# Kernel optimization log

Measured on AMD Instinct MI355X. Metric: run time of the kernel, lower is better.

## Reference

```python
import jax, jax.numpy as jnp
import numpy as np

E = 8            # moe_num_experts
FFN = 8192       # ffn_hidden_size
D = 2048         # d_model
B, T = 1, 4096


def setup_inputs() -> dict:
    key = jax.random.key(0)
    k1, k2, k3, k4 = jax.random.split(key, 4)
    x = jax.random.normal(k1, (B, T, D), dtype=jnp.float32)
    # params stored flat as (E*FFN, D), as in the flax module
    w1 = jax.random.normal(k2, (E * FFN, D), dtype=jnp.float32) * 0.02
    v1 = jax.random.normal(k3, (E * FFN, D), dtype=jnp.float32) * 0.02
    w2 = jax.random.normal(k4, (E * FFN, D), dtype=jnp.float32) * 0.02
    return {"x": x, "w1": w1, "v1": v1, "w2": w2, "expert_idx": 3}


def reference(x, w1, v1, w2, expert_idx):
    # select this expert's weight slabs: (FFN, D) each
    expert_shape = (E, FFN, D)
    ew1 = w1.reshape(expert_shape)[expert_idx]
    ev1 = v1.reshape(expert_shape)[expert_idx]
    ew2 = w2.reshape(expert_shape)[expert_idx]
    # gate and up projections: [B,T,D] x [D,FFN] -> [B,T,FFN]
    x1 = jnp.einsum('btd,fd->btf', x, ew1)
    x2 = jnp.einsum('btd,fd->btf', x, ev1)
    h = jax.nn.silu(x1) * x2
    # down projection (note: matmul with ew2, i.e. contraction over FFN)
    out = jnp.einsum('btf,fd->btd', h, ew2)
    return out
```

## Files before the change

kernel.cpp:

```cpp
#include <hip/hip_runtime.h>

#define E_NUM 8
#define FFN_DIM 8192
#define D_DIM 2048
#define T_DIM 4096

using bf16x8 = __attribute__((ext_vector_type(8))) short;
using f32x4  = __attribute__((ext_vector_type(4))) float;
using u16x8  = __attribute__((ext_vector_type(8))) unsigned short;

__device__ __forceinline__ unsigned short f2bf(float f) {
  union { float f; unsigned int u; } v; v.f = f;
  unsigned int u = v.u;
  unsigned int r = (u + 0x7FFFu + ((u >> 16) & 1u)) >> 16;
  return (unsigned short)r;
}

__device__ __forceinline__ void gload16(const unsigned short* g, const unsigned short* l) {
  __builtin_amdgcn_global_load_lds(
      (const __attribute__((address_space(1))) void*)g,
      (__attribute__((address_space(3))) void*)l, 16, 0, 0);
}

__global__ __launch_bounds__(512) void prep4_kernel(
    const float* __restrict__ x,  const float* __restrict__ w1,
    const float* __restrict__ v1, const float* __restrict__ w2,
    const int* __restrict__ eidx,
    unsigned short* __restrict__ Xb,  unsigned short* __restrict__ W1b,
    unsigned short* __restrict__ V1b, unsigned short* __restrict__ W2T) {
  __shared__ unsigned short tile[64][72];
  const long slab = (long)FFN_DIM * D_DIM;
  const int tid = threadIdx.x;

  if (blockIdx.y == 3) {
    const float* src = w2 + (long)(*eidx) * slab;
    int d0 = (blockIdx.x & 31) << 6;
    int f0 = (blockIdx.x >> 5) << 6;
#pragma unroll
    for (int p = 0; p < 2; ++p) {
      int f = p * 32 + (tid >> 4);
      int dc = (tid & 15) * 4;
      float4 v = *(const float4*)(src + (long)(f0 + f) * D_DIM + d0 + dc);
      tile[f][dc + 0] = f2bf(v.x); tile[f][dc + 1] = f2bf(v.y);
      tile[f][dc + 2] = f2bf(v.z); tile[f][dc + 3] = f2bf(v.w);
    }
    __syncthreads();
    int d = tid >> 3;
    int fc = (tid & 7) * 8;
    u16x8 o;
#pragma unroll
    for (int j = 0; j < 8; ++j) o[j] = tile[fc + j][d];
    *(u16x8*)(W2T + (long)(d0 + d) * FFN_DIM + f0 + fc) = o;
    return;
  }

  const float* src;
  unsigned short* dst;
  long n;
  if (blockIdx.y == 0)      { src = w1 + (long)(*eidx) * slab; dst = W1b; n = slab; }
  else if (blockIdx.y == 1) { src = v1 + (long)(*eidx) * slab; dst = V1b; n = slab; }
  else                      { src = x;                          dst = Xb;  n = (long)T_DIM * D_DIM; }
  long stride = (long)gridDim.x * blockDim.x;
  for (long i = (long)blockIdx.x * blockDim.x + tid; i * 8 < n; i += stride) {
    long e = i * 8;
    const float4* p = (const float4*)(src + e);
    float4 f0 = p[0], f1 = p[1];
    u16x8 o;
    o[0] = f2bf(f0.x); o[1] = f2bf(f0.y); o[2] = f2bf(f0.z); o[3] = f2bf(f0.w);
    o[4] = f2bf(f1.x); o[5] = f2bf(f1.y); o[6] = f2bf(f1.z); o[7] = f2bf(f1.w);
    *(u16x8*)(dst + e) = o;
  }
}

#define VMCNT8 asm volatile("s_waitcnt vmcnt(8)" ::: "memory")
#define VMCNT5 asm volatile("s_waitcnt vmcnt(5)" ::: "memory")
#define VMCNT0 asm volatile("s_waitcnt vmcnt(0)" ::: "memory")
#define BAR asm volatile("s_waitcnt lgkmcnt(0)\n\ts_barrier" ::: "memory")
#define PRIO1 __builtin_amdgcn_s_setprio(1)
#define PRIO0 __builtin_amdgcn_s_setprio(0)

__global__ __launch_bounds__(512, 1) void gemm1_silu(
    const unsigned short* __restrict__ Xb,
    const unsigned short* __restrict__ W1b,
    const unsigned short* __restrict__ V1b,
    unsigned short* __restrict__ Hb) {
  __shared__ __align__(16) unsigned short sA[2 * 16384];
  __shared__ __align__(16) unsigned short sB1[2 * 8192];
  __shared__ __align__(16) unsigned short sB2[2 * 8192];

  const int tid = threadIdx.x;
  const int wv = tid >> 6, l = tid & 63;
  const int wm = wv >> 2, wn = wv & 3;
  const int kq = l >> 4, lr = l & 15;
  const int bsw = (blockIdx.x & 7) * 128 + (blockIdx.x >> 3);
  const int m0 = (bsw >> 6) << 8;
  const int n0 = (bsw & 63) << 7;

  const int rsub = tid >> 3;
  const int sslot8 = ((tid & 7) ^ ((tid >> 3) & 7)) << 3;
  const unsigned short* gA  = Xb  + (long)(m0 + rsub) * D_DIM + sslot8;
  const unsigned short* gB1 = W1b + (long)(n0 + rsub) * D_DIM + sslot8;
  const unsigned short* gB2 = V1b + (long)(n0 + rsub) * D_DIM + sslot8;

#define STG1(gbase, r_, tc_, lbase) \
  gload16((gbase) + (long)((r_) * 64) * D_DIM + (tc_), (lbase) + (r_) * 4096 + wv * 512)

  int aoffA[4], aoffB[4], boff[2];
#pragma unroll
  for (int j = 0; j < 4; ++j) {
    int rowA = wm * 64 + j * 16 + lr;
    aoffA[j] = rowA * 64 + ((kq ^ (rowA & 7)) << 3);
    int rowB = 128 + wm * 64 + j * 16 + lr;
    aoffB[j] = rowB * 64 + ((kq ^ (rowB & 7)) << 3);
  }
#pragma unroll
  for (int g = 0; g < 2; ++g) {
    int row = wn * 32 + g * 16 + lr;
    boff[g] = row * 64 + ((kq ^ (row & 7)) << 3);
  }

  f32x4 acc1[8][2], acc2[8][2];
  f32x4 z = {0.f, 0.f, 0.f, 0.f};
#pragma unroll
  for (int f = 0; f < 8; ++f)
#pragma unroll
    for (int g = 0; g < 2; ++g) { acc1[f][g] = z; acc2[f][g] = z; }

  bf16x8 aA[4][2], aB[4][2], b1[2][2], b2[2][2];

  STG1(gB1, 0, 0, sB1); STG1(gB1, 1, 0, sB1);
  STG1(gA, 0, 0, sA); STG1(gA, 1, 0, sA); STG1(gA, 2, 0, sA); STG1(gA, 3, 0, sA);
  STG1(gB2, 0, 0, sB2); STG1(gB2, 1, 0, sB2);
  STG1(gB1, 0, 64, sB1 + 8192); STG1(gB1, 1, 64, sB1 + 8192);
  STG1(gA, 0, 64, sA + 16384); STG1(gA, 1, 64, sA + 16384);
  STG1(gA, 2, 64, sA + 16384); STG1(gA, 3, 64, sA + 16384);
  STG1(gB2, 0, 64, sB2 + 8192); STG1(gB2, 1, 64, sB2 + 8192);
  VMCNT8;
  BAR;
#pragma unroll
  for (int j = 0; j < 4; ++j) {
    aA[j][0] = *(const bf16x8*)(sA + aoffA[j]);
    aA[j][1] = *(const bf16x8*)(sA + (aoffA[j] ^ 32));
  }
#pragma unroll
  for (int g = 0; g < 2; ++g) {
    b1[g][0] = *(const bf16x8*)(sB1 + boff[g]);
    b1[g][1] = *(const bf16x8*)(sB1 + (boff[g] ^ 32));
  }
  BAR;

  const int NT = D_DIM / 64;
  for (int t = 0; t < NT; ++t) {
    const int db = t & 1, nx = db ^ 1;
    const unsigned short* Acur  = sA  + db * 16384;
    const unsigned short* Anxt  = sA  + nx * 16384;
    const unsigned short* B1nxt = sB1 + nx * 8192;
    const unsigned short* B2cur = sB2 + db * 8192;
    unsigned short* AcurW  = (unsigned short*)sA  + db * 16384;
    unsigned short* B1curW = (unsigned short*)sB1 + db * 8192;
    unsigned short* B2curW = (unsigned short*)sB2 + db * 8192;
    const int p1ok = (t + 1 < NT), p2ok = (t + 2 < NT);
    const int tc2 = (t + 2) << 6;

#pragma unroll
    for (int j = 0; j < 4; ++j) {
      aB[j][0] = *(const bf16x8*)(Acur + aoffB[j]);
      aB[j][1] = *(const bf16x8*)(Acur + (aoffB[j] ^ 32));
    }
    if (p2ok) { STG1(gB1, 0, tc2, B1curW); STG1(gB1, 1, tc2, B1curW); }
    PRIO1;
#pragma unroll
    for (int j = 0; j < 4; ++j)
#pragma unroll
      for (int g = 0; g < 2; ++g) {
        acc1[j][g] = __builtin_amdgcn_mfma_f32_16x16x32_bf16(aA[j][0], b1[g][0], acc1[j][g], 0, 0, 0);
        acc1[j][g] = __builtin_amdgcn_mfma_f32_16x16x32_bf16(aA[j][1], b1[g][1], acc1[j][g], 0, 0, 0);
      }
    PRIO0;
    BAR;

#pragma unroll
    for (int g = 0; g < 2; ++g) {
      b2[g][0] = *(const bf16x8*)(B2cur + boff[g]);
      b2[g][1] = *(const bf16x8*)(B2cur + (boff[g] ^ 32));
    }
    if (p2ok) { STG1(gA, 0, tc2, AcurW); STG1(gA, 1, tc2, AcurW); STG1(gA, 2, tc2, AcurW); }
    PRIO1;
#pragma unroll
    for (int j = 0; j < 4; ++j)
#pragma unroll
      for (int g = 0; g < 2; ++g) {
        acc1[4 + j][g] = __builtin_amdgcn_mfma_f32_16x16x32_bf16(aB[j][0], b1[g][0], acc1[4 + j][g], 0, 0, 0);
        acc1[4 + j][g] = __builtin_amdgcn_mfma_f32_16x16x32_bf16(aB[j][1], b1[g][1], acc1[4 + j][g], 0, 0, 0);
      }
    PRIO0;
    if (p2ok) { VMCNT5; } else if (p1ok) { VMCNT0; }
    BAR;

    if (p2ok) { STG1(gA, 3, tc2, AcurW); STG1(gB2, 0, tc2, B2curW); STG1(gB2, 1, tc2, B2curW); }
    PRIO1;
#pragma unroll
    for (int j = 0; j < 4; ++j)
#pragma unroll
      for (int g = 0; g < 2; ++g) {
        acc2[j][g] = __builtin_amdgcn_mfma_f32_16x16x32_bf16(aA[j][0], b2[g][0], acc2[j][g], 0, 0, 0);
        acc2[j][g] = __builtin_amdgcn_mfma_f32_16x16x32_bf16(aA[j][1], b2[g][1], acc2[j][g], 0, 0, 0);
      }
    PRIO0;
    if (p1ok) {
#pragma unroll
      for (int j = 0; j < 4; ++j) {
        aA[j][0] = *(const bf16x8*)(Anxt + aoffA[j]);
        aA[j][1] = *(const bf16x8*)(Anxt + (aoffA[j] ^ 32));
      }
    }
    BAR;

    PRIO1;
#pragma unroll
    for (int j = 0; j < 4; ++j)
#pragma unroll
      for (int g = 0; g < 2; ++g) {
        acc2[4 + j][g] = __builtin_amdgcn_mfma_f32_16x16x32_bf16(aB[j][0], b2[g][0], acc2[4 + j][g], 0, 0, 0);
        acc2[4 + j][g] = __builtin_amdgcn_mfma_f32_16x16x32_bf16(aB[j][1], b2[g][1], acc2[4 + j][g], 0, 0, 0);
      }
    PRIO0;
    if (p1ok) {
#pragma unroll
      for (int g = 0; g < 2; ++g) {
        b1[g][0] = *(const bf16x8*)(B1nxt + boff[g]);
        b1[g][1] = *(const bf16x8*)(B1nxt + (boff[g] ^ 32));
      }
    }
    BAR;
  }

#pragma unroll
  for (int f = 0; f < 8; ++f)
#pragma unroll
    for (int g = 0; g < 2; ++g)
#pragma unroll
      for (int r = 0; r < 4; ++r) {
        int row = m0 + (f >> 2) * 128 + wm * 64 + (f & 3) * 16 + kq * 4 + r;
        int col = n0 + wn * 32 + g * 16 + lr;
        float x1 = acc1[f][g][r], x2 = acc2[f][g][r];
        float hv = x1 / (1.f + __expf(-x1)) * x2;
        Hb[(long)row * FFN_DIM + col] = f2bf(hv);
      }
#undef STG1
}

__global__ __launch_bounds__(256, 2) void gemm2(
    const unsigned short* __restrict__ Hb,
    const unsigned short* __restrict__ W2T,
    float* __restrict__ out) {
  __shared__ __align__(16) unsigned short sA[2 * 8192];
  __shared__ __align__(16) unsigned short sB[2 * 8192];

  const int tid = threadIdx.x;
  const int wv = tid >> 6, l = tid & 63;
  const int wm = wv >> 1, wn = wv & 1;
  const int kq = l >> 4, lr = l & 15;
  const int bsw = (blockIdx.x & 7) * 64 + (blockIdx.x >> 3);
  const int m0 = (bsw >> 4) << 7;
  const int n0 = (bsw & 15) << 7;

  const int rsub = tid >> 3;
  const int sslot8 = ((tid & 7) ^ (rsub & 7)) << 3;
  const unsigned short* gA = Hb  + (long)(m0 + rsub) * FFN_DIM + sslot8;
  const unsigned short* gB = W2T + (long)(n0 + rsub) * FFN_DIM + sslot8;

#define STG2(gbase, r_, tc_, lbase) \
  gload16((gbase) + (long)((r_) * 32) * FFN_DIM + (tc_), (lbase) + (r_) * 2048 + wv * 512)

  int aoff[4], boff[4];
#pragma unroll
  for (int f = 0; f < 4; ++f) {
    int row = wm * 64 + f * 16 + lr;
    aoff[f] = row * 64 + ((kq ^ (row & 7)) << 3);
  }
#pragma unroll
  for (int g = 0; g < 4; ++g) {
    int row = wn * 64 + g * 16 + lr;
    boff[g] = row * 64 + ((kq ^ (row & 7)) << 3);
  }

  f32x4 acc[4][4];
  f32x4 z = {0.f, 0.f, 0.f, 0.f};
#pragma unroll
  for (int f = 0; f < 4; ++f)
#pragma unroll
    for (int g = 0; g < 4; ++g) acc[f][g] = z;

  STG2(gA, 0, 0, sA); STG2(gA, 1, 0, sA); STG2(gA, 2, 0, sA); STG2(gA, 3, 0, sA);
  STG2(gB, 0, 0, sB); STG2(gB, 1, 0, sB); STG2(gB, 2, 0, sB); STG2(gB, 3, 0, sB);
  STG2(gA, 0, 64, sA + 8192); STG2(gA, 1, 64, sA + 8192);
  STG2(gA, 2, 64, sA + 8192); STG2(gA, 3, 64, sA + 8192);
  STG2(gB, 0, 64, sB + 8192); STG2(gB, 1, 64, sB + 8192);
  STG2(gB, 2, 64, sB + 8192); STG2(gB, 3, 64, sB + 8192);
  VMCNT8;
  BAR;

  const int NT = FFN_DIM / 64;
  for (int t = 0; t < NT; ++t) {
    const int cur = t & 1;
    const unsigned short* Ac = sA + cur * 8192;
    const unsigned short* Bc = sB + cur * 8192;
    unsigned short* AcW = (unsigned short*)sA + cur * 8192;
    unsigned short* BcW = (unsigned short*)sB + cur * 8192;
    bf16x8 af[4][2], bf_[4][2];

#pragma unroll
    for (int f = 0; f < 4; ++f) {
      af[f][0] = *(const bf16x8*)(Ac + aoff[f]);
      af[f][1] = *(const bf16x8*)(Ac + (aoff[f] ^ 32));
    }
#pragma unroll
    for (int g = 0; g < 4; ++g) {
      bf_[g][0] = *(const bf16x8*)(Bc + boff[g]);
      bf_[g][1] = *(const bf16x8*)(Bc + (boff[g] ^ 32));
    }
    PRIO1;
#pragma unroll
    for (int f = 0; f < 4; ++f)
#pragma unroll
      for (int g = 0; g < 4; ++g) {
        acc[f][g] = __builtin_amdgcn_mfma_f32_16x16x32_bf16(af[f][0], bf_[g][0], acc[f][g], 0, 0, 0);
        acc[f][g] = __builtin_amdgcn_mfma_f32_16x16x32_bf16(af[f][1], bf_[g][1], acc[f][g], 0, 0, 0);
      }
    PRIO0;
    BAR;

    if (t + 2 < NT) {
      const int tc2 = (t + 2) << 6;
      STG2(gA, 0, tc2, AcW); STG2(gA, 1, tc2, AcW);
      STG2(gA, 2, tc2, AcW); STG2(gA, 3, tc2, AcW);
      STG2(gB, 0, tc2, BcW); STG2(gB, 1, tc2, BcW);
      STG2(gB, 2, tc2, BcW); STG2(gB, 3, tc2, BcW);
      VMCNT8;
    } else if (t + 1 < NT) {
      VMCNT0;
    }
    BAR;
  }

#pragma unroll
  for (int f = 0; f < 4; ++f)
#pragma unroll
    for (int g = 0; g < 4; ++g)
#pragma unroll
      for (int r = 0; r < 4; ++r) {
        int row = m0 + wm * 64 + f * 16 + kq * 4 + r;
        int col = n0 + wn * 64 + g * 16 + lr;
        out[(long)row * D_DIM + col] = acc[f][g][r];
      }
#undef STG2
}

extern "C" void kernel_launch(void* const* d_in, const int* in_sizes, int n_in,
                              void* d_out, int out_size, void* d_ws, size_t ws_size,
                              hipStream_t stream) {
  const float* x  = (const float*)d_in[0];
  const float* w1 = (const float*)d_in[1];
  const float* v1 = (const float*)d_in[2];
  const float* w2 = (const float*)d_in[3];
  const int* eidx = (const int*)d_in[4];

  char* ws = (char*)d_ws;
  unsigned short* Xb  = (unsigned short*)(ws);
  unsigned short* W1b = (unsigned short*)(ws + (16l << 20));
  unsigned short* V1b = (unsigned short*)(ws + (48l << 20));
  unsigned short* W2T = (unsigned short*)(ws + (80l << 20));
  unsigned short* Hb  = (unsigned short*)(ws + (112l << 20));
  float* out = (float*)d_out;

  prep4_kernel<<<dim3(4096, 4), 512, 0, stream>>>(x, w1, v1, w2, eidx, Xb, W1b, V1b, W2T);
  gemm1_silu<<<1024, 512, 0, stream>>>(Xb, W1b, V1b, Hb);
  gemm2<<<512, 256, 0, stream>>>(Hb, W2T, out);
}
```

Baseline: 440.1 us.

## Shrink gemm1 tile to 128x64 with 256 threads and simpler double buffering

The gate/up GEMM kernel moves from 512-thread blocks with 256x128 tiles and a phase-interleaved 4-barrier pipeline to 256-thread blocks with 128x64 tiles, two blocks per CU, 4096 blocks, and a single compute phase per k-step followed by bulk prefetch. This makes the schedule simpler, raises occupancy and spreads work over more blocks. In exchange, arithmetic intensity per tile drops, so more global/L2 traffic is needed per FLOP, and the hand-tuned overlap of LDS reads with MFMA is lost.

```diff
diff --git a/kernel.cpp b/kernel.cpp
--- a/kernel.cpp
+++ b/kernel.cpp
@@ -73,45 +73,42 @@
 }
 
 #define VMCNT8 asm volatile("s_waitcnt vmcnt(8)" ::: "memory")
-#define VMCNT5 asm volatile("s_waitcnt vmcnt(5)" ::: "memory")
 #define VMCNT0 asm volatile("s_waitcnt vmcnt(0)" ::: "memory")
 #define BAR asm volatile("s_waitcnt lgkmcnt(0)\n\ts_barrier" ::: "memory")
 #define PRIO1 __builtin_amdgcn_s_setprio(1)
 #define PRIO0 __builtin_amdgcn_s_setprio(0)
 
-__global__ __launch_bounds__(512, 1) void gemm1_silu(
+__global__ __launch_bounds__(256, 2) void gemm1_silu(
     const unsigned short* __restrict__ Xb,
     const unsigned short* __restrict__ W1b,
     const unsigned short* __restrict__ V1b,
     unsigned short* __restrict__ Hb) {
-  __shared__ __align__(16) unsigned short sA[2 * 16384];
-  __shared__ __align__(16) unsigned short sB1[2 * 8192];
-  __shared__ __align__(16) unsigned short sB2[2 * 8192];
+  __shared__ __align__(16) unsigned short sA[2 * 8192];
+  __shared__ __align__(16) unsigned short sB1[2 * 4096];
+  __shared__ __align__(16) unsigned short sB2[2 * 4096];
 
   const int tid = threadIdx.x;
   const int wv = tid >> 6, l = tid & 63;
-  const int wm = wv >> 2, wn = wv & 3;
+  const int wm = wv >> 1, wn = wv & 1;
   const int kq = l >> 4, lr = l & 15;
-  const int bsw = (blockIdx.x & 7) * 128 + (blockIdx.x >> 3);
-  const int m0 = (bsw >> 6) << 8;
-  const int n0 = (bsw & 63) << 7;
+  const int bsw = (blockIdx.x & 7) * 512 + (blockIdx.x >> 3);
+  const int m0 = (bsw & 31) << 7;
+  const int n0 = (bsw >> 5) << 6;
 
   const int rsub = tid >> 3;
-  const int sslot8 = ((tid & 7) ^ ((tid >> 3) & 7)) << 3;
+  const int sslot8 = ((tid & 7) ^ (rsub & 7)) << 3;
   const unsigned short* gA  = Xb  + (long)(m0 + rsub) * D_DIM + sslot8;
   const unsigned short* gB1 = W1b + (long)(n0 + rsub) * D_DIM + sslot8;
   const unsigned short* gB2 = V1b + (long)(n0 + rsub) * D_DIM + sslot8;
 
 #define STG1(gbase, r_, tc_, lbase) \
-  gload16((gbase) + (long)((r_) * 64) * D_DIM + (tc_), (lbase) + (r_) * 4096 + wv * 512)
-
-  int aoffA[4], aoffB[4], boff[2];
+  gload16((gbase) + (long)((r_) * 32) * D_DIM + (tc_), (lbase) + (r_) * 2048 + wv * 512)
+
+  int aoff[4], boff[2];
 #pragma unroll
   for (int j = 0; j < 4; ++j) {
-    int rowA = wm * 64 + j * 16 + lr;
-    aoffA[j] = rowA * 64 + ((kq ^ (rowA & 7)) << 3);
-    int rowB = 128 + wm * 64 + j * 16 + lr;
-    aoffB[j] = rowB * 64 + ((kq ^ (rowB & 7)) << 3);
+    int row = wm * 64 + j * 16 + lr;
+    aoff[j] = row * 64 + ((kq ^ (row & 7)) << 3);
   }
 #pragma unroll
   for (int g = 0; g < 2; ++g) {
@@ -119,55 +116,46 @@
     boff[g] = row * 64 + ((kq ^ (row & 7)) << 3);
   }
 
-  f32x4 acc1[8][2], acc2[8][2];
+  f32x4 acc1[4][2], acc2[4][2];
   f32x4 z = {0.f, 0.f, 0.f, 0.f};
 #pragma unroll
-  for (int f = 0; f < 8; ++f)
-#pragma unroll
-    for (int g = 0; g < 2; ++g) { acc1[f][g] = z; acc2[f][g] = z; }
-
-  bf16x8 aA[4][2], aB[4][2], b1[2][2], b2[2][2];
-
+  for (int j = 0; j < 4; ++j)
+#pragma unroll
+    for (int g = 0; g < 2; ++g) { acc1[j][g] = z; acc2[j][g] = z; }
+
+  STG1(gA, 0, 0, sA); STG1(gA, 1, 0, sA); STG1(gA, 2, 0, sA); STG1(gA, 3, 0, sA);
   STG1(gB1, 0, 0, sB1); STG1(gB1, 1, 0, sB1);
-  STG1(gA, 0, 0, sA); STG1(gA, 1, 0, sA); STG1(gA, 2, 0, sA); STG1(gA, 3, 0, sA);
   STG1(gB2, 0, 0, sB2); STG1(gB2, 1, 0, sB2);
-  STG1(gB1, 0, 64, sB1 + 8192); STG1(gB1, 1, 64, sB1 + 8192);
-  STG1(gA, 0, 64, sA + 16384); STG1(gA, 1, 64, sA + 16384);
-  STG1(gA, 2, 64, sA + 16384); STG1(gA, 3, 64, sA + 16384);
-  STG1(gB2, 0, 64, sB2 + 8192); STG1(gB2, 1, 64, sB2 + 8192);
+  STG1(gA, 0, 64, sA + 8192); STG1(gA, 1, 64, sA + 8192);
+  STG1(gA, 2, 64, sA + 8192); STG1(gA, 3, 64, sA + 8192);
+  STG1(gB1, 0, 64, sB1 + 4096); STG1(gB1, 1, 64, sB1 + 4096);
+  STG1(gB2, 0, 64, sB2 + 4096); STG1(gB2, 1, 64, sB2 + 4096);
   VMCNT8;
   BAR;
-#pragma unroll
-  for (int j = 0; j < 4; ++j) {
-    aA[j][0] = *(const bf16x8*)(sA + aoffA[j]);
-    aA[j][1] = *(const bf16x8*)(sA + (aoffA[j] ^ 32));
-  }
-#pragma unroll
-  for (int g = 0; g < 2; ++g) {
-    b1[g][0] = *(const bf16x8*)(sB1 + boff[g]);
-    b1[g][1] = *(const bf16x8*)(sB1 + (boff[g] ^ 32));
-  }
-  BAR;
 
   const int NT = D_DIM / 64;
   for (int t = 0; t < NT; ++t) {
-    const int db = t & 1, nx = db ^ 1;
-    const unsigned short* Acur  = sA  + db * 16384;
-    const unsigned short* Anxt  = sA  + nx * 16384;
-    const unsigned short* B1nxt = sB1 + nx * 8192;
-    const unsigned short* B2cur = sB2 + db * 8192;
-    unsigned short* AcurW  = (unsigned short*)sA  + db * 16384;
-    unsigned short* B1curW = (unsigned short*)sB1 + db * 8192;
-    unsigned short* B2curW = (unsigned short*)sB2 + db * 8192;
-    const int p1ok = (t + 1 < NT), p2ok = (t + 2 < NT);
-    const int tc2 = (t + 2) << 6;
+    const int cur = t & 1;
+    const unsigned short* Ac  = sA  + cur * 8192;
+    const unsigned short* B1c = sB1 + cur * 4096;
+    const unsigned short* B2c = sB2 + cur * 4096;
+    unsigned short* AcW  = (unsigned short*)sA  + cur * 8192;
+    unsigned short* B1cW = (unsigned short*)sB1 + cur * 4096;
+    unsigned short* B2cW = (unsigned short*)sB2 + cur * 4096;
+    bf16x8 aA[4][2], b1[2][2], b2[2][2];
 
 #pragma unroll
     for (int j = 0; j < 4; ++j) {
-      aB[j][0] = *(const bf16x8*)(Acur + aoffB[j]);
-      aB[j][1] = *(const bf16x8*)(Acur + (aoffB[j] ^ 32));
-    }
-    if (p2ok) { STG1(gB1, 0, tc2, B1curW); STG1(gB1, 1, tc2, B1curW); }
+      aA[j][0] = *(const bf16x8*)(Ac + aoff[j]);
+      aA[j][1] = *(const bf16x8*)(Ac + (aoff[j] ^ 32));
+    }
+#pragma unroll
+    for (int g = 0; g < 2; ++g) {
+      b1[g][0] = *(const bf16x8*)(B1c + boff[g]);
+      b1[g][1] = *(const bf16x8*)(B1c + (boff[g] ^ 32));
+      b2[g][0] = *(const bf16x8*)(B2c + boff[g]);
+      b2[g][1] = *(const bf16x8*)(B2c + (boff[g] ^ 32));
+    }
     PRIO1;
 #pragma unroll
     for (int j = 0; j < 4; ++j)
@@ -175,75 +163,34 @@
       for (int g = 0; g < 2; ++g) {
         acc1[j][g] = __builtin_amdgcn_mfma_f32_16x16x32_bf16(aA[j][0], b1[g][0], acc1[j][g], 0, 0, 0);
         acc1[j][g] = __builtin_amdgcn_mfma_f32_16x16x32_bf16(aA[j][1], b1[g][1], acc1[j][g], 0, 0, 0);
-      }
-    PRIO0;
-    BAR;
-
-#pragma unroll
-    for (int g = 0; g < 2; ++g) {
-      b2[g][0] = *(const bf16x8*)(B2cur + boff[g]);
-      b2[g][1] = *(const bf16x8*)(B2cur + (boff[g] ^ 32));
-    }
-    if (p2ok) { STG1(gA, 0, tc2, AcurW); STG1(gA, 1, tc2, AcurW); STG1(gA, 2, tc2, AcurW); }
-    PRIO1;
-#pragma unroll
-    for (int j = 0; j < 4; ++j)
-#pragma unroll
-      for (int g = 0; g < 2; ++g) {
-        acc1[4 + j][g] = __builtin_amdgcn_mfma_f32_16x16x32_bf16(aB[j][0], b1[g][0], acc1[4 + j][g], 0, 0, 0);
-        acc1[4 + j][g] = __builtin_amdgcn_mfma_f32_16x16x32_bf16(aB[j][1], b1[g][1], acc1[4 + j][g], 0, 0, 0);
-      }
-    PRIO0;
-    if (p2ok) { VMCNT5; } else if (p1ok) { VMCNT0; }
-    BAR;
-
-    if (p2ok) { STG1(gA, 3, tc2, AcurW); STG1(gB2, 0, tc2, B2curW); STG1(gB2, 1, tc2, B2curW); }
-    PRIO1;
-#pragma unroll
-    for (int j = 0; j < 4; ++j)
-#pragma unroll
-      for (int g = 0; g < 2; ++g) {
         acc2[j][g] = __builtin_amdgcn_mfma_f32_16x16x32_bf16(aA[j][0], b2[g][0], acc2[j][g], 0, 0, 0);
         acc2[j][g] = __builtin_amdgcn_mfma_f32_16x16x32_bf16(aA[j][1], b2[g][1], acc2[j][g], 0, 0, 0);
       }
     PRIO0;
-    if (p1ok) {
-#pragma unroll
-      for (int j = 0; j < 4; ++j) {
-        aA[j][0] = *(const bf16x8*)(Anxt + aoffA[j]);
-        aA[j][1] = *(const bf16x8*)(Anxt + (aoffA[j] ^ 32));
-      }
-    }
     BAR;
 
-    PRIO1;
-#pragma unroll
-    for (int j = 0; j < 4; ++j)
-#pragma unroll
-      for (int g = 0; g < 2; ++g) {
-        acc2[4 + j][g] = __builtin_amdgcn_mfma_f32_16x16x32_bf16(aB[j][0], b2[g][0], acc2[4 + j][g], 0, 0, 0);
-        acc2[4 + j][g] = __builtin_amdgcn_mfma_f32_16x16x32_bf16(aB[j][1], b2[g][1], acc2[4 + j][g], 0, 0, 0);
-      }
-    PRIO0;
-    if (p1ok) {
-#pragma unroll
-      for (int g = 0; g < 2; ++g) {
-        b1[g][0] = *(const bf16x8*)(B1nxt + boff[g]);
-        b1[g][1] = *(const bf16x8*)(B1nxt + (boff[g] ^ 32));
-      }
+    if (t + 2 < NT) {
+      const int tc2 = (t + 2) << 6;
+      STG1(gA, 0, tc2, AcW); STG1(gA, 1, tc2, AcW);
+      STG1(gA, 2, tc2, AcW); STG1(gA, 3, tc2, AcW);
+      STG1(gB1, 0, tc2, B1cW); STG1(gB1, 1, tc2, B1cW);
+      STG1(gB2, 0, tc2, B2cW); STG1(gB2, 1, tc2, B2cW);
+      VMCNT8;
+    } else if (t + 1 < NT) {
+      VMCNT0;
     }
     BAR;
   }
 
 #pragma unroll
-  for (int f = 0; f < 8; ++f)
+  for (int j = 0; j < 4; ++j)
 #pragma unroll
     for (int g = 0; g < 2; ++g)
 #pragma unroll
       for (int r = 0; r < 4; ++r) {
-        int row = m0 + (f >> 2) * 128 + wm * 64 + (f & 3) * 16 + kq * 4 + r;
+        int row = m0 + wm * 64 + j * 16 + kq * 4 + r;
         int col = n0 + wn * 32 + g * 16 + lr;
-        float x1 = acc1[f][g][r], x2 = acc2[f][g][r];
+        float x1 = acc1[j][g][r], x2 = acc2[j][g][r];
         float hv = x1 / (1.f + __expf(-x1)) * x2;
         Hb[(long)row * FFN_DIM + col] = f2bf(hv);
       }
@@ -375,6 +322,6 @@
   float* out = (float*)d_out;
 
   prep4_kernel<<<dim3(4096, 4), 512, 0, stream>>>(x, w1, v1, w2, eidx, Xb, W1b, V1b, W2T);
-  gemm1_silu<<<1024, 512, 0, stream>>>(Xb, W1b, V1b, Hb);
+  gemm1_silu<<<4096, 256, 0, stream>>>(Xb, W1b, V1b, Hb);
   gemm2<<<512, 256, 0, stream>>>(Hb, W2T, out);
 }
```

Measured after the change: 566.1 us. 28.6% more time.
